# Kernel tuning notes

Measured on AMD Instinct MI355X. Metric: run time of the kernel, lower is better.

The kernel has to match this reference:

```python
import jax, jax.numpy as jnp
import numpy as np

NQ = 4
NL = 3
HEADS = 8

_H = jnp.asarray(np.array([[1, 1], [1, -1]], np.complex64) / np.sqrt(2.0))
_X = jnp.asarray(np.array([[0, 1], [1, 0]], np.complex64))
_Y = jnp.asarray(np.array([[0, -1j], [1j, 0]], np.complex64))
_Z = jnp.asarray(np.array([[1, 0], [0, -1]], np.complex64))
_CNOT = jnp.asarray(np.array([[1, 0, 0, 0], [0, 1, 0, 0], [0, 0, 0, 1], [0, 0, 1, 0]], np.complex64))


def _rx(t):
    c = jnp.cos(t / 2).astype(jnp.complex64)
    s = (-1j * jnp.sin(t / 2)).astype(jnp.complex64)
    return jnp.stack([jnp.stack([c, s]), jnp.stack([s, c])])


def _ry(t):
    c = jnp.cos(t / 2).astype(jnp.complex64)
    s = jnp.sin(t / 2).astype(jnp.complex64)
    return jnp.stack([jnp.stack([c, -s]), jnp.stack([s, c])])


def _rz(t):
    e = jnp.exp((-0.5j) * t).astype(jnp.complex64)
    z = jnp.zeros((), jnp.complex64)
    return jnp.stack([jnp.stack([e, z]), jnp.stack([z, jnp.conj(e)])])


def _crx(t):
    # control-RX in |control,target> basis
    return jnp.eye(4, dtype=jnp.complex64).at[2:, 2:].set(_rx(t))


def _ap1(psi, U, q):
    # apply 2x2 gate U on qubit axis q of psi:(2,2,2,2)
    return jnp.moveaxis(jnp.tensordot(U, psi, axes=[[1], [q]]), 0, q)


def _ap2(psi, U, q1, q2):
    p = jnp.moveaxis(psi, (q1, q2), (0, 1)).reshape(4, 4)
    p = (U @ p).reshape(2, 2, 2, 2)
    return jnp.moveaxis(p, (0, 1), (q1, q2))


def _expv(psi, P, q):
    return jnp.real(jnp.vdot(psi, _ap1(psi, P, q)))


def _circuit(inp, w, ew, gam, bet):
    # inp:(4,)  w,ew:(3,4)  gam,bet:(3,)  -> (12,) expvals Z,X,Y
    psi = jnp.zeros((16,), jnp.complex64).at[0].set(1.0).reshape(2, 2, 2, 2)
    for i in range(NQ):  # AngleEmbedding(rotation='Y')
        psi = _ap1(psi, _ry(inp[i]), i)
    for L in range(NL):
        for i in range(NQ):
            psi = _ap1(psi, _rx(w[L, i]), i)
            psi = _ap1(psi, _ry(w[L, i]), i)
            psi = _ap1(psi, _rz(w[L, i]), i)
        for i in range(NQ):  # CRX entangling ring
            psi = _ap2(psi, _crx(ew[L, i]), i, (i + 1) % NQ)
        # Grover diffusion
        for q in range(NQ):
            psi = _ap1(psi, _H, q)
        for q in range(NQ):
            psi = _ap1(psi, _X, q)
        psi = _ap1(psi, _H, NQ - 1)
        psi = psi.at[1, 1, 1, :].set(psi[1, 1, 1, ::-1])  # CCCX ctrl=[0,1,2] tgt=3
        psi = _ap1(psi, _H, NQ - 1)
        for q in range(NQ):
            psi = _ap1(psi, _X, q)
        for q in range(NQ):
            psi = _ap1(psi, _H, q)
        # QAOA cost + mixer
        for i in range(NQ - 1):
            psi = _ap2(psi, _CNOT, i, i + 1)
            psi = _ap1(psi, _rz(gam[L]), i + 1)
            psi = _ap2(psi, _CNOT, i, i + 1)
        for q in range(NQ):
            psi = _ap1(psi, _rx(bet[L]), q)
    meas = [_expv(psi, _Z, q) for q in range(NQ)]
    meas += [_expv(psi, _X, q) for q in range(NQ)]
    meas += [_expv(psi, _Y, q) for q in range(NQ)]
    return jnp.stack(meas)


_vqc = jax.vmap(_circuit, in_axes=(0, None, None, None, None))


def _layernorm(x, g, b, eps=1e-5):
    mu = jnp.mean(x, -1, keepdims=True)
    var = jnp.mean((x - mu) ** 2, -1, keepdims=True)
    return (x - mu) * jax.lax.rsqrt(var + eps) * g + b


def _qtransform(xf, Wp, bp, ln_g, ln_b, w, ew, gam, bet):
    p = jnp.tanh(xf @ Wp.T + bp)  # (BS,4)
    p = _layernorm(p, ln_g, ln_b)
    return _vqc(p, w, ew, gam, bet)  # (BS,12)


def setup_inputs() -> dict:
    key = jax.random.key(0)
    ks = jax.random.split(key, 32)
    B, S, Hd = 4, 1024, 512
    d = {"x": jax.random.normal(ks[0], (B, S, Hd), jnp.float32)}
    d["Wp"] = jax.random.normal(ks[1], (NQ, Hd), jnp.float32) * 0.05
    d["bp"] = jnp.zeros((NQ,), jnp.float32)
    d["ln_g"] = jnp.ones((NQ,), jnp.float32)
    d["ln_b"] = jnp.zeros((NQ,), jnp.float32)
    i = 2
    for pfx in ["q", "k", "v"]:
        d[pfx + "w"] = 0.01 * jax.random.normal(ks[i], (NL, NQ), jnp.float32)
        d[pfx + "e"] = 0.01 * jax.random.normal(ks[i + 1], (NL, NQ), jnp.float32)
        d[pfx + "g"] = 0.01 * jax.random.normal(ks[i + 2], (NL,), jnp.float32)
        d[pfx + "b"] = 0.01 * jax.random.normal(ks[i + 3], (NL,), jnp.float32)
        i += 4
    fused = 3 * NQ
    d["Wq"] = jax.random.normal(ks[i], (Hd, fused), jnp.float32) * 0.2
    d["bq"] = jnp.zeros((Hd,), jnp.float32)
    d["Wk"] = jax.random.normal(ks[i + 1], (Hd, fused), jnp.float32) * 0.2
    d["bk"] = jnp.zeros((Hd,), jnp.float32)
    d["Wv"] = jax.random.normal(ks[i + 2], (Hd, fused), jnp.float32) * 0.2
    d["bv"] = jnp.zeros((Hd,), jnp.float32)
    d["Wo"] = jax.random.normal(ks[i + 3], (Hd, Hd), jnp.float32) * 0.05
    d["bo"] = jnp.zeros((Hd,), jnp.float32)
    return d


def reference(x, Wp, bp, ln_g, ln_b, qw, qe, qg, qb, kw, ke, kg, kb, vw, ve, vg, vb,
              Wq, bq, Wk, bk, Wv, bv, Wo, bo):
    B, S, Hd = x.shape
    hd = Hd // HEADS
    xf = x.reshape(B * S, Hd)
    tq = _qtransform(xf, Wp, bp, ln_g, ln_b, qw, qe, qg, qb)
    tk = _qtransform(xf, Wp, bp, ln_g, ln_b, kw, ke, kg, kb)
    tv = _qtransform(xf, Wp, bp, ln_g, ln_b, vw, ve, vg, vb)
    q = (tq @ Wq.T + bq).reshape(B, S, HEADS, hd)
    k = (tk @ Wk.T + bk).reshape(B, S, HEADS, hd)
    v = (tv @ Wv.T + bv).reshape(B, S, HEADS, hd)
    scale = float(hd) ** 0.5
    attn = jax.nn.softmax(jnp.einsum('bqhd,bkhd->bhqk', q, k) / scale, axis=-1)
    out = jnp.einsum('bhqk,bkhd->bqhd', attn, v).reshape(B, S, Hd)
    return out @ Wo.T + bo
```

## Files before the change

### kernel.cpp

```cpp
#include <hip/hip_runtime.h>
#include <hip/hip_bf16.h>
#include <math.h>

#define NROWS 4096
#define HD 512
#define HEADS 8
#define HDD 64
#define SEQ 1024
#define QSCALE 0.18033688011112042f

typedef unsigned short u16;
typedef unsigned int u32;
typedef unsigned long long u64;
typedef __attribute__((ext_vector_type(8))) short sh8;
typedef __attribute__((ext_vector_type(4))) float f4;

__device__ __forceinline__ f4 mfma16(sh8 a, sh8 b, f4 c) {
  return __builtin_amdgcn_mfma_f32_16x16x32_bf16(a, b, c, 0, 0, 0);
}

__device__ __forceinline__ u16 f2bf(float x) {
  union { float f; unsigned u; } v; v.f = x;
  unsigned r = v.u + 0x7fff + ((v.u >> 16) & 1);
  return (u16)(r >> 16);
}

__device__ __forceinline__ u32 cvt_pk_bf16(float lo, float hi) {
  u32 r;
  asm("v_cvt_pk_bf16_f32 %0, %1, %2" : "=v"(r) : "v"(lo), "v"(hi));
  return r;
}

#define SWZA(r, cb) ((((r) * 128) + (cb)) ^ (((r) & 7) << 4))

__global__ __launch_bounds__(256) void k_prep(
    const float* __restrict__ qw, const float* __restrict__ qe,
    const float* __restrict__ qg, const float* __restrict__ qb,
    const float* __restrict__ kw, const float* __restrict__ ke,
    const float* __restrict__ kg, const float* __restrict__ kb,
    const float* __restrict__ vw, const float* __restrict__ ve,
    const float* __restrict__ vg, const float* __restrict__ vb,
    float* __restrict__ Mout) {
  const int c = blockIdx.x;
  const int tid = threadIdx.x;
  __shared__ float aC[32], aS[32];
  __shared__ float GT[60][8];
  __shared__ int   GM[60][2];
  __shared__ float PF[3][16][2];
  __shared__ float SR[16][17], SI[16][17];
  __shared__ float TS[16], TI[16];
  __shared__ float Ur[256], Ui[256];

  const float* w = (c == 0) ? qw : (c == 1) ? kw : vw;
  const float* e = (c == 0) ? qe : (c == 1) ? ke : ve;
  const float* g = (c == 0) ? qg : (c == 1) ? kg : vg;
  const float* b = (c == 0) ? qb : (c == 1) ? kb : vb;

  if (tid < 30) {
    float ang = (tid < 12) ? w[tid] : (tid < 24) ? e[tid - 12]
               : (tid < 27) ? g[tid - 24] : b[tid - 27];
    float s_, c_;
    sincosf(0.5f * ang, &s_, &c_);
    aC[tid] = c_; aS[tid] = s_;
  }
  __syncthreads();

  if (tid < 60) {
    int L = tid / 20, s5 = tid % 20;
    int typ, aidx, M, C;
    if (s5 < 12) {
      int q = s5 / 3; typ = s5 % 3; aidx = L * 4 + q; M = 8 >> q; C = 0;
    } else if (s5 < 16) {
      int q = s5 - 12; typ = 0; aidx = 12 + L * 4 + q;
      C = 8 >> q; M = 8 >> ((q + 1) & 3);
    } else {
      int q = s5 - 16; typ = 0; aidx = 27 + L; M = 8 >> q; C = 0;
    }
    float cc = aC[aidx], ss = aS[aidx];
    float u0r = cc, u0i = 0.f, u1r = 0.f, u1i = 0.f,
          u2r = 0.f, u2i = 0.f, u3r = cc, u3i = 0.f;
    if (typ == 0)      { u1i = -ss; u2i = -ss; }
    else if (typ == 1) { u1r = -ss; u2r = ss; }
    else               { u0i = -ss; u3i = ss; }
    GT[tid][0] = u0r; GT[tid][1] = u0i; GT[tid][2] = u1r; GT[tid][3] = u1i;
    GT[tid][4] = u2r; GT[tid][5] = u2i; GT[tid][6] = u3r; GT[tid][7] = u3i;
    GM[tid][0] = M; GM[tid][1] = C;
  }
  if (tid >= 64 && tid < 112) {
    int idx = tid - 64, L = idx >> 4, a = idx & 15;
    float cg = aC[24 + L], sg = aS[24 + L];
    float c2 = cg * cg - sg * sg, s2 = 2.f * cg * sg;
    float c3 = cg * c2 - sg * s2, s3 = cg * s2 + sg * c2;
    int u = (a ^ (a >> 1)) & 7;
    int n = (u & 1) + ((u >> 1) & 1) + ((u >> 2) & 1);
    PF[L][a][0] = (n == 0 || n == 3) ? c3 : cg;
    PF[L][a][1] = (n == 0) ? -s3 : (n == 1) ? -sg : (n == 2) ? sg : s3;
  }
  for (int i = tid; i < 256; i += 256) {
    SR[i >> 4][i & 15] = (i >> 4) == (i & 15) ? 1.f : 0.f;
    SI[i >> 4][i & 15] = 0.f;
  }
  __syncthreads();

  const int p = tid >> 4, col = tid & 15;
  for (int L = 0; L < 3; ++L) {
    for (int s5 = 0; s5 < 16; ++s5) {
      if (tid < 128) {
        int gi = L * 20 + s5;
        const float* u = GT[gi];
        int M = GM[gi][0], C = GM[gi][1];
        int lo = p & (M - 1);
        int a = ((p - lo) << 1) | lo;
        int bb = a | M;
        bool act = (C == 0) | ((a & C) != 0);
        float ar = SR[a][col], ai = SI[a][col];
        float br = SR[bb][col], bi = SI[bb][col];
        float nar = u[0]*ar - u[1]*ai + u[2]*br - u[3]*bi;
        float nai = u[0]*ai + u[1]*ar + u[2]*bi + u[3]*br;
        float nbr = u[4]*ar - u[5]*ai + u[6]*br - u[7]*bi;
        float nbi = u[4]*ai + u[5]*ar + u[6]*bi + u[7]*br;
        SR[a][col]  = act ? nar : ar;  SI[a][col]  = act ? nai : ai;
        SR[bb][col] = act ? nbr : br;  SI[bb][col] = act ? nbi : bi;
      }
      __syncthreads();
    }
    if (tid < 16) {
      float sR = 0.f, sI = 0.f;
      for (int a = 0; a < 16; ++a) { sR += SR[a][tid]; sI += SI[a][tid]; }
      TS[tid] = sR * 0.125f; TI[tid] = sI * 0.125f;
    }
    __syncthreads();
    if (tid < 128) {
      for (int k = 0; k < 2; ++k) {
        int a = 2 * p + k;
        float vr = SR[a][col] - TS[col];
        float vi = SI[a][col] - TI[col];
        float pc = PF[L][a][0], ps = PF[L][a][1];
        SR[a][col] = vr * pc - vi * ps;
        SI[a][col] = vr * ps + vi * pc;
      }
    }
    __syncthreads();
    for (int s5 = 16; s5 < 20; ++s5) {
      if (tid < 128) {
        int gi = L * 20 + s5;
        const float* u = GT[gi];
        int M = GM[gi][0];
        int lo = p & (M - 1);
        int a = ((p - lo) << 1) | lo;
        int bb = a | M;
        float ar = SR[a][col], ai = SI[a][col];
        float br = SR[bb][col], bi = SI[bb][col];
        SR[a][col]  = u[0]*ar - u[1]*ai + u[2]*br - u[3]*bi;
        SI[a][col]  = u[0]*ai + u[1]*ar + u[2]*bi + u[3]*br;
        SR[bb][col] = u[4]*ar - u[5]*ai + u[6]*br - u[7]*bi;
        SI[bb][col] = u[4]*ai + u[5]*ar + u[6]*bi + u[7]*br;
      }
      __syncthreads();
    }
  }

  for (int i = tid; i < 256; i += 256) {
    Ur[i] = SR[i >> 4][i & 15];
    Ui[i] = SI[i >> 4][i & 15];
  }
  __syncthreads();

  if (tid < 192) {
    const int j = tid >> 4, a = tid & 15;
    const int typ = j >> 2;
    const int Mm = 8 >> (j & 3);
    float ax[4] = {0.f,0.f,0.f,0.f}, ay[4] = {0.f,0.f,0.f,0.f},
          az[4] = {0.f,0.f,0.f,0.f}, aw[4] = {0.f,0.f,0.f,0.f};
#pragma clang loop unroll_count(4)
    for (int k = 0; k < 16; ++k) {
      float uar = Ur[k * 16 + a], uai = Ui[k * 16 + a];
      int k2; float cR, cI;
      if (typ == 0)      { k2 = k;      float z = (k & Mm) ? -1.f : 1.f; cR = z*uar; cI = z*uai; }
      else if (typ == 1) { k2 = k ^ Mm; cR = uar; cI = uai; }
      else               { k2 = k ^ Mm; float sg = (k & Mm) ? 1.f : -1.f; cR = sg*uai; cI = -sg*uar; }
      const float* ur2 = Ur + k2 * 16;
      const float* ui2 = Ui + k2 * 16;
#pragma unroll
      for (int i = 0; i < 4; ++i) {
        ax[i] += cR * ur2[i*4+0] + cI * ui2[i*4+0];
        ay[i] += cR * ur2[i*4+1] + cI * ui2[i*4+1];
        az[i] += cR * ur2[i*4+2] + cI * ui2[i*4+2];
        aw[i] += cR * ur2[i*4+3] + cI * ui2[i*4+3];
      }
    }
    float* dst = Mout + ((c * 12 + j) * 16 + a) * 16;
#pragma unroll
    for (int i = 0; i < 4; ++i)
      ((float4*)dst)[i] = make_float4(ax[i], ay[i], az[i], aw[i]);
  }
}

__global__ __launch_bounds__(256) void k_front(const float* __restrict__ x,
    const float* __restrict__ Wp, const float* __restrict__ bp,
    const float* __restrict__ ln_g, const float* __restrict__ ln_b,
    const float* __restrict__ Mg,
    const float* __restrict__ Wq, const float* __restrict__ bq,
    const float* __restrict__ Wk, const float* __restrict__ bk,
    const float* __restrict__ Wv, const float* __restrict__ bv,
    u16* __restrict__ Qo, u16* __restrict__ Ko, u16* __restrict__ Vto) {
  const int rb = blockIdx.x;
  const int tid = threadIdx.x;
  const int w = tid >> 6, lane = tid & 63;
  __shared__ float pl[4][4];
  __shared__ float psil[4][16];
  __shared__ float tt[3][4][12];

  {
    const float* xr = x + (rb * 4 + w) * HD + lane * 8;
    float4 xa = *(const float4*)xr, xb = *(const float4*)(xr + 4);
    float acc[4];
#pragma unroll
    for (int j = 0; j < 4; ++j) {
      const float* wr = Wp + j * HD + lane * 8;
      float4 wa = *(const float4*)wr, wb = *(const float4*)(wr + 4);
      acc[j] = xa.x*wa.x + xa.y*wa.y + xa.z*wa.z + xa.w*wa.w
             + xb.x*wb.x + xb.y*wb.y + xb.z*wb.z + xb.w*wb.w;
    }
#pragma unroll
    for (int j = 0; j < 4; ++j)
#pragma unroll
      for (int off = 32; off >= 1; off >>= 1)
        acc[j] += __shfl_xor(acc[j], off);
    if (lane == 0) {
      float v0 = tanhf(acc[0] + bp[0]);
      float v1 = tanhf(acc[1] + bp[1]);
      float v2 = tanhf(acc[2] + bp[2]);
      float v3 = tanhf(acc[3] + bp[3]);
      float mu = 0.25f * (v0 + v1 + v2 + v3);
      float d0 = v0 - mu, d1 = v1 - mu, d2 = v2 - mu, d3 = v3 - mu;
      float inv = rsqrtf(0.25f * (d0*d0 + d1*d1 + d2*d2 + d3*d3) + 1e-5f);
      pl[w][0] = d0 * inv * ln_g[0] + ln_b[0];
      pl[w][1] = d1 * inv * ln_g[1] + ln_b[1];
      pl[w][2] = d2 * inv * ln_g[2] + ln_b[2];
      pl[w][3] = d3 * inv * ln_g[3] + ln_b[3];
    }
  }
  __syncthreads();

  if (tid < 4) {
    float cs[4], sn[4];
    sincosf(0.5f * pl[tid][0], &sn[0], &cs[0]);
    sincosf(0.5f * pl[tid][1], &sn[1], &cs[1]);
    sincosf(0.5f * pl[tid][2], &sn[2], &cs[2]);
    sincosf(0.5f * pl[tid][3], &sn[3], &cs[3]);
    float q01[4] = {cs[0]*cs[1], cs[0]*sn[1], sn[0]*cs[1], sn[0]*sn[1]};
    float q23[4] = {cs[2]*cs[3], cs[2]*sn[3], sn[2]*cs[3], sn[2]*sn[3]};
#pragma unroll
    for (int a = 0; a < 16; ++a) psil[tid][a] = q01[a >> 2] * q23[a & 3];
  }
  __syncthreads();

  if (tid < 144) {
    const int c = tid / 48, rem = tid - c * 48, j = rem >> 2, r = rem & 3;
    float psi[16];
#pragma unroll
    for (int a = 0; a < 16; ++a) psi[a] = psil[r][a];
    const float4* Mj = (const float4*)(Mg + (c * 12 + j) * 256);
    float y = 0.f;
#pragma unroll
    for (int a = 0; a < 16; ++a) {
      float rsum = 0.f;
#pragma unroll
      for (int i = 0; i < 4; ++i) {
        float4 m4 = Mj[a * 4 + i];
        rsum += m4.x*psi[i*4] + m4.y*psi[i*4+1] + m4.z*psi[i*4+2] + m4.w*psi[i*4+3];
      }
      y += psi[a] * rsum;
    }
    tt[c][r][j] = y;
  }
  __syncthreads();

  const int o0 = tid * 2;
  const int b = rb >> 8, ss0 = (rb & 255) * 4;
  const int h = o0 >> 6, d = o0 & 63;
#pragma unroll
  for (int c = 0; c < 3; ++c) {
    const float* W  = (c == 0) ? Wq : (c == 1) ? Wk : Wv;
    const float* bb = (c == 0) ? bq : (c == 1) ? bk : bv;
    float4 w0a = *(const float4*)(W + o0 * 12);
    float4 w0b = *(const float4*)(W + o0 * 12 + 4);
    float4 w0c = *(const float4*)(W + o0 * 12 + 8);
    float4 w1a = *(const float4*)(W + o0 * 12 + 12);
    float4 w1b = *(const float4*)(W + o0 * 12 + 16);
    float4 w1c = *(const float4*)(W + o0 * 12 + 20);
    float b0 = bb[o0], b1 = bb[o0 + 1];
    float r0[4], r1[4];
#pragma unroll
    for (int r = 0; r < 4; ++r) {
      const float* t = tt[c][r];
      r0[r] = b0 + t[0]*w0a.x + t[1]*w0a.y + t[2]*w0a.z + t[3]*w0a.w
                 + t[4]*w0b.x + t[5]*w0b.y + t[6]*w0b.z + t[7]*w0b.w
                 + t[8]*w0c.x + t[9]*w0c.y + t[10]*w0c.z + t[11]*w0c.w;
      r1[r] = b1 + t[0]*w1a.x + t[1]*w1a.y + t[2]*w1a.z + t[3]*w1a.w
                 + t[4]*w1b.x + t[5]*w1b.y + t[6]*w1b.z + t[7]*w1b.w
                 + t[8]*w1c.x + t[9]*w1c.y + t[10]*w1c.z + t[11]*w1c.w;
    }
    if (c == 0) {
      u16* qrow = Qo + ((b * HEADS + h) * SEQ + ss0) * HDD + d;
#pragma unroll
      for (int r = 0; r < 4; ++r)
        *(u32*)(qrow + r * HDD) =
            (u32)f2bf(r0[r] * QSCALE) | ((u32)f2bf(r1[r] * QSCALE) << 16);
    } else if (c == 1) {
      u16* krow = Ko + ((b * HEADS + h) * SEQ + ss0) * HDD + d;
#pragma unroll
      for (int r = 0; r < 4; ++r)
        *(u32*)(krow + r * HDD) = (u32)f2bf(r0[r]) | ((u32)f2bf(r1[r]) << 16);
    } else {
      u64 v0 = (u64)((u32)f2bf(r0[0]) | ((u32)f2bf(r0[1]) << 16)) |
               ((u64)((u32)f2bf(r0[2]) | ((u32)f2bf(r0[3]) << 16)) << 32);
      u64 v1 = (u64)((u32)f2bf(r1[0]) | ((u32)f2bf(r1[1]) << 16)) |
               ((u64)((u32)f2bf(r1[2]) | ((u32)f2bf(r1[3]) << 16)) << 32);
      *(u64*)(Vto + (b * 512 + o0) * SEQ + ss0) = v0;
      *(u64*)(Vto + (b * 512 + o0 + 1) * SEQ + ss0) = v1;
    }
  }
}

__global__ __launch_bounds__(256) void k_attn_mfma(const u16* __restrict__ Q,
    const u16* __restrict__ K, const u16* __restrict__ Vt,
    float* __restrict__ Op, float* __restrict__ Lp) {
  const int bh = blockIdx.y, qt = blockIdx.x, ks = blockIdx.z;
  const int tid = threadIdx.x, w = tid >> 6, l = tid & 63;
  const int lr = l & 15, lh = l >> 4;

  __shared__ u16 Kl[2][64 * 64];
  __shared__ u16 Vl[2][64 * 64];
  __shared__ u16 Pl[4][16 * 64];

  const u16* Qb = Q + (bh * SEQ + qt * 64) * HDD;
  const u16* Kb = K + bh * SEQ * HDD;
  const u16* Vb = Vt + bh * HDD * SEQ;
  const int CH0 = ks * 8;
  u16* Plw = Pl[w];

  sh8 qf[2];
#pragma unroll
  for (int kk = 0; kk < 2; ++kk)
    qf[kk] = *(const sh8*)(Qb + (w * 16 + lr) * HDD + kk * 32 + lh * 8);

  f4 oacc[4];
  float lsum = 0.f;
#pragma unroll
  for (int n = 0; n < 4; ++n) oacc[n] = (f4){0.f, 0.f, 0.f, 0.f};

  sh8 kreg[2], vreg[2];

#define STAGE_LOAD(ch) { \
    _Pragma("unroll") \
    for (int i = 0; i < 2; ++i) { \
      int idx = i * 256 + tid; \
      kreg[i] = *(const sh8*)(Kb + ((ch) * 64 + (idx >> 3)) * HDD + (idx & 7) * 8); \
      vreg[i] = *(const sh8*)(Vb + (idx >> 3) * SEQ + (ch) * 64 + (idx & 7) * 8); \
    } }
#define STAGE_WRITE(buf) { \
    _Pragma("unroll") \
    for (int i = 0; i < 2; ++i) { \
      int idx = i * 256 + tid; \
      *(sh8*)((char*)Kl[buf] + SWZA(idx >> 3, (idx & 7) * 16)) = kreg[i]; \
      *(sh8*)((char*)Vl[buf] + SWZA(idx >> 3, (idx & 7) * 16)) = vreg[i]; \
    } }

  STAGE_LOAD(CH0)
  STAGE_WRITE(0)
  __syncthreads();

  for (int it = 0; it < 8; ++it) {
    const int cur = it & 1;
    if (it < 7) STAGE_LOAD(CH0 + it + 1)

    f4 sacc[4];
#pragma unroll
    for (int n = 0; n < 4; ++n) sacc[n] = (f4){0.f, 0.f, 0.f, 0.f};
    __builtin_amdgcn_s_setprio(1);
#pragma unroll
    for (int kk = 0; kk < 2; ++kk) {
#pragma unroll
      for (int n = 0; n < 4; ++n) {
        sh8 kf = *(const sh8*)((const char*)Kl[cur] + SWZA(n * 16 + lr, kk * 64 + lh * 16));
        sacc[n] = mfma16(kf, qf[kk], sacc[n]);
      }
    }
    __builtin_amdgcn_s_setprio(0);

#pragma unroll
    for (int n = 0; n < 4; ++n) {
      float p0 = exp2f(sacc[n][0]);
      float p1 = exp2f(sacc[n][1]);
      float p2 = exp2f(sacc[n][2]);
      float p3 = exp2f(sacc[n][3]);
      lsum += (p0 + p1) + (p2 + p3);
      u32 w0 = cvt_pk_bf16(p0, p1);
      u32 w1 = cvt_pk_bf16(p2, p3);
      *(uint2*)((char*)Plw + SWZA(lr, n * 32 + lh * 8)) = make_uint2(w0, w1);
    }

    __builtin_amdgcn_s_setprio(1);
#pragma unroll
    for (int kk = 0; kk < 2; ++kk) {
      sh8 pf = *(const sh8*)((const char*)Plw + SWZA(lr, kk * 64 + lh * 16));
#pragma unroll
      for (int n = 0; n < 4; ++n) {
        sh8 vf = *(const sh8*)((const char*)Vl[cur] + SWZA(n * 16 + lr, kk * 64 + lh * 16));
        oacc[n] = mfma16(pf, vf, oacc[n]);
      }
    }
    __builtin_amdgcn_s_setprio(0);

    if (it < 7) STAGE_WRITE(cur ^ 1)
    __syncthreads();
  }
#undef STAGE_LOAD
#undef STAGE_WRITE

  lsum += __shfl_xor(lsum, 16);
  lsum += __shfl_xor(lsum, 32);

  const int bb = bh >> 3, h = bh & 7;
#pragma unroll
  for (int r = 0; r < 4; ++r) {
    int row = qt * 64 + w * 16 + lh * 4 + r;
    float* orow = Op + ((ks * NROWS + bb * SEQ + row) * HD) + h * 64;
#pragma unroll
    for (int n = 0; n < 4; ++n)
      orow[n * 16 + lr] = oacc[n][r];
  }
  if (l < 16)
    Lp[(ks * 32 + bh) * SEQ + qt * 64 + w * 16 + lr] = lsum;
}

__global__ __launch_bounds__(256) void k_combine(const float* __restrict__ Op,
    const float* __restrict__ Lp, u16* __restrict__ ab) {
  const int idx = (blockIdx.x * 256 + threadIdx.x) * 8;
  const int row = idx >> 9, col = idx & 511;
  const int bb = row >> 10, srow = row & 1023, h = col >> 6;
  float l0 = Lp[(bb * 8 + h) * SEQ + srow];
  float l1 = Lp[(32 + bb * 8 + h) * SEQ + srow];
  float linv = 1.f / (l0 + l1);
  const float* o0 = Op + idx;
  const float* o1 = o0 + NROWS * HD;
  float4 a0 = *(const float4*)o0, a1 = *(const float4*)(o0 + 4);
  float4 b0 = *(const float4*)o1, b1 = *(const float4*)(o1 + 4);
  uint4 v;
  v.x = cvt_pk_bf16((a0.x + b0.x) * linv, (a0.y + b0.y) * linv);
  v.y = cvt_pk_bf16((a0.z + b0.z) * linv, (a0.w + b0.w) * linv);
  v.z = cvt_pk_bf16((a1.x + b1.x) * linv, (a1.y + b1.y) * linv);
  v.w = cvt_pk_bf16((a1.z + b1.z) * linv, (a1.w + b1.w) * linv);
  *(uint4*)(ab + idx) = v;
}

__global__ __launch_bounds__(256) void k_oproj_mfma(const u16* __restrict__ A,
    const float* __restrict__ W, const float* __restrict__ bo,
    float* __restrict__ out) {
  const int nb = blockIdx.x, ob = blockIdx.y;
  const int tid = threadIdx.x, w = tid >> 6, l = tid & 63;
  const int lr = l & 15, lh = l >> 4;
  __shared__ u16 Al[64 * 64];
  __shared__ u16 Wl[64 * 64];
  f4 acc[4];
#pragma unroll
  for (int n = 0; n < 4; ++n) acc[n] = (f4){0.f, 0.f, 0.f, 0.f};
  for (int ch = 0; ch < 8; ++ch) {
    __syncthreads();
#pragma unroll
    for (int i = 0; i < 2; ++i) {
      int idx = i * 256 + tid;
      int r = idx >> 3, c8 = idx & 7;
      *(sh8*)((char*)Al + SWZA(r, c8 * 16)) =
          *(const sh8*)(A + (nb * 64 + r) * HD + ch * 64 + c8 * 8);
      const float* wp = W + (ob * 64 + r) * HD + ch * 64 + c8 * 8;
      float4 f0 = *(const float4*)wp;
      float4 f1 = *(const float4*)(wp + 4);
      uint4 wv;
      wv.x = cvt_pk_bf16(f0.x, f0.y);
      wv.y = cvt_pk_bf16(f0.z, f0.w);
      wv.z = cvt_pk_bf16(f1.x, f1.y);
      wv.w = cvt_pk_bf16(f1.z, f1.w);
      *(uint4*)((char*)Wl + SWZA(r, c8 * 16)) = wv;
    }
    __syncthreads();
#pragma unroll
    for (int kk = 0; kk < 2; ++kk) {
      sh8 af = *(const sh8*)((const char*)Al + SWZA(w * 16 + lr, kk * 64 + lh * 16));
#pragma unroll
      for (int n = 0; n < 4; ++n) {
        sh8 wf = *(const sh8*)((const char*)Wl + SWZA(n * 16 + lr, kk * 64 + lh * 16));
        acc[n] = mfma16(af, wf, acc[n]);
      }
    }
  }
#pragma unroll
  for (int r = 0; r < 4; ++r) {
    int row = nb * 64 + w * 16 + lh * 4 + r;
#pragma unroll
    for (int n = 0; n < 4; ++n) {
      int col = ob * 64 + n * 16 + lr;
      out[row * HD + col] = acc[n][r] + bo[col];
    }
  }
}

extern "C" void kernel_launch(void* const* d_in, const int* in_sizes, int n_in,
                              void* d_out, int out_size, void* d_ws, size_t ws_size,
                              hipStream_t stream) {
  const float* x    = (const float*)d_in[0];
  const float* Wp   = (const float*)d_in[1];
  const float* bp   = (const float*)d_in[2];
  const float* ln_g = (const float*)d_in[3];
  const float* ln_b = (const float*)d_in[4];
  const float* qw   = (const float*)d_in[5];
  const float* qe   = (const float*)d_in[6];
  const float* qg   = (const float*)d_in[7];
  const float* qb_  = (const float*)d_in[8];
  const float* kw   = (const float*)d_in[9];
  const float* ke   = (const float*)d_in[10];
  const float* kg   = (const float*)d_in[11];
  const float* kb_  = (const float*)d_in[12];
  const float* vw   = (const float*)d_in[13];
  const float* ve   = (const float*)d_in[14];
  const float* vg   = (const float*)d_in[15];
  const float* vb_  = (const float*)d_in[16];
  const float* Wq   = (const float*)d_in[17];
  const float* bq   = (const float*)d_in[18];
  const float* Wk   = (const float*)d_in[19];
  const float* bk   = (const float*)d_in[20];
  const float* Wv   = (const float*)d_in[21];
  const float* bv   = (const float*)d_in[22];
  const float* Wo   = (const float*)d_in[23];
  const float* bo   = (const float*)d_in[24];

  float* ws   = (float*)d_ws;
  float* Mbuf = ws;
  u16* qb  = (u16*)(Mbuf + 9216);
  u16* kb  = qb + 32 * SEQ * HDD;
  u16* vtb = kb + 32 * SEQ * HDD;
  float* Opart = (float*)(vtb + 32 * SEQ * HDD);
  float* Lpart = Opart + 2 * NROWS * HD;
  u16* ab = (u16*)(Lpart + 2 * 32 * SEQ);

  k_prep<<<3, 256, 0, stream>>>(qw, qe, qg, qb_, kw, ke, kg, kb_,
                                vw, ve, vg, vb_, Mbuf);
  k_front<<<NROWS / 4, 256, 0, stream>>>(x, Wp, bp, ln_g, ln_b, Mbuf,
                                         Wq, bq, Wk, bk, Wv, bv, qb, kb, vtb);
  dim3 ga(SEQ / 64, 32, 2);
  k_attn_mfma<<<ga, 256, 0, stream>>>(qb, kb, vtb, Opart, Lpart);
  k_combine<<<NROWS * HD / 2048, 256, 0, stream>>>(Opart, Lpart, ab);
  dim3 go(NROWS / 64, HD / 64);
  k_oproj_mfma<<<go, 256, 0, stream>>>(ab, Wo, bo, (float*)d_out);
}
```

Before: 80.79 us.

## Drop split-K attention and fuse normalization into attention epilogue

The attention kernel no longer splits the key sequence into two halves. Each block now loops over all 16 key chunks, then normalizes by the row sum and writes bf16 output directly, so the separate combine kernel and its fp32 partial buffers go away. Block indices are remapped so that blocks with consecutive IDs are spread across heads, which is likely aimed at XCD/L2 locality. In exchange the grid halves to 512 blocks, each running twice as many serial iterations, which lowers parallelism.

```diff
diff --git a/kernel.cpp b/kernel.cpp
--- a/kernel.cpp
+++ b/kernel.cpp
@@ -326,8 +326,9 @@
 
 __global__ __launch_bounds__(256) void k_attn_mfma(const u16* __restrict__ Q,
     const u16* __restrict__ K, const u16* __restrict__ Vt,
-    float* __restrict__ Op, float* __restrict__ Lp) {
-  const int bh = blockIdx.y, qt = blockIdx.x, ks = blockIdx.z;
+    u16* __restrict__ Ob) {
+  const int lin = (blockIdx.x & 7) * 64 + (blockIdx.x >> 3);
+  const int bh = lin >> 4, qt = lin & 15;
   const int tid = threadIdx.x, w = tid >> 6, l = tid & 63;
   const int lr = l & 15, lh = l >> 4;
 
@@ -338,7 +339,6 @@
   const u16* Qb = Q + (bh * SEQ + qt * 64) * HDD;
   const u16* Kb = K + bh * SEQ * HDD;
   const u16* Vb = Vt + bh * HDD * SEQ;
-  const int CH0 = ks * 8;
   u16* Plw = Pl[w];
 
   sh8 qf[2];
@@ -368,13 +368,13 @@
       *(sh8*)((char*)Vl[buf] + SWZA(idx >> 3, (idx & 7) * 16)) = vreg[i]; \
     } }
 
-  STAGE_LOAD(CH0)
+  STAGE_LOAD(0)
   STAGE_WRITE(0)
   __syncthreads();
 
-  for (int it = 0; it < 8; ++it) {
+  for (int it = 0; it < 16; ++it) {
     const int cur = it & 1;
-    if (it < 7) STAGE_LOAD(CH0 + it + 1)
+    if (it < 15) STAGE_LOAD(it + 1)
 
     f4 sacc[4];
 #pragma unroll
@@ -414,7 +414,7 @@
     }
     __builtin_amdgcn_s_setprio(0);
 
-    if (it < 7) STAGE_WRITE(cur ^ 1)
+    if (it < 15) STAGE_WRITE(cur ^ 1)
     __syncthreads();
   }
 #undef STAGE_LOAD
@@ -427,33 +427,12 @@
 #pragma unroll
   for (int r = 0; r < 4; ++r) {
     int row = qt * 64 + w * 16 + lh * 4 + r;
-    float* orow = Op + ((ks * NROWS + bb * SEQ + row) * HD) + h * 64;
+    float inv = 1.f / __shfl(lsum, lh * 4 + r);
+    u16* orow = Ob + (bb * SEQ + row) * HD + h * 64;
 #pragma unroll
     for (int n = 0; n < 4; ++n)
-      orow[n * 16 + lr] = oacc[n][r];
-  }
-  if (l < 16)
-    Lp[(ks * 32 + bh) * SEQ + qt * 64 + w * 16 + lr] = lsum;
-}
-
-__global__ __launch_bounds__(256) void k_combine(const float* __restrict__ Op,
-    const float* __restrict__ Lp, u16* __restrict__ ab) {
-  const int idx = (blockIdx.x * 256 + threadIdx.x) * 8;
-  const int row = idx >> 9, col = idx & 511;
-  const int bb = row >> 10, srow = row & 1023, h = col >> 6;
-  float l0 = Lp[(bb * 8 + h) * SEQ + srow];
-  float l1 = Lp[(32 + bb * 8 + h) * SEQ + srow];
-  float linv = 1.f / (l0 + l1);
-  const float* o0 = Op + idx;
-  const float* o1 = o0 + NROWS * HD;
-  float4 a0 = *(const float4*)o0, a1 = *(const float4*)(o0 + 4);
-  float4 b0 = *(const float4*)o1, b1 = *(const float4*)(o1 + 4);
-  uint4 v;
-  v.x = cvt_pk_bf16((a0.x + b0.x) * linv, (a0.y + b0.y) * linv);
-  v.y = cvt_pk_bf16((a0.z + b0.z) * linv, (a0.w + b0.w) * linv);
-  v.z = cvt_pk_bf16((a1.x + b1.x) * linv, (a1.y + b1.y) * linv);
-  v.w = cvt_pk_bf16((a1.z + b1.z) * linv, (a1.w + b1.w) * linv);
-  *(uint4*)(ab + idx) = v;
+      orow[n * 16 + lr] = f2bf(oacc[n][r] * inv);
+  }
 }
 
 __global__ __launch_bounds__(256) void k_oproj_mfma(const u16* __restrict__ A,
@@ -541,17 +520,13 @@
   u16* qb  = (u16*)(Mbuf + 9216);
   u16* kb  = qb + 32 * SEQ * HDD;
   u16* vtb = kb + 32 * SEQ * HDD;
-  float* Opart = (float*)(vtb + 32 * SEQ * HDD);
-  float* Lpart = Opart + 2 * NROWS * HD;
-  u16* ab = (u16*)(Lpart + 2 * 32 * SEQ);
+  u16* ab  = vtb + 32 * SEQ * HDD;
 
   k_prep<<<3, 256, 0, stream>>>(qw, qe, qg, qb_, kw, ke, kg, kb_,
                                 vw, ve, vg, vb_, Mbuf);
   k_front<<<NROWS / 4, 256, 0, stream>>>(x, Wp, bp, ln_g, ln_b, Mbuf,
                                          Wq, bq, Wk, bk, Wv, bv, qb, kb, vtb);
-  dim3 ga(SEQ / 64, 32, 2);
-  k_attn_mfma<<<ga, 256, 0, stream>>>(qb, kb, vtb, Opart, Lpart);
-  k_combine<<<NROWS * HD / 2048, 256, 0, stream>>>(Opart, Lpart, ab);
+  k_attn_mfma<<<512, 256, 0, stream>>>(qb, kb, vtb, ab);
   dim3 go(NROWS / 64, HD / 64);
   k_oproj_mfma<<<go, 256, 0, stream>>>(ab, Wo, bo, (float*)d_out);
 }
```

After: 74.09 us. 8.3% less time.
